# Kernel optimization log

Hardware: AMD Instinct MI355X
Metric: run time of the kernel (lower is better)

Reference implementation:

```python
import jax, jax.numpy as jnp
import numpy as np

B, S, D, H = 4, 2048, 1024, 16
DK = D // H

def setup_inputs() -> dict:
    key = jax.random.key(0)
    ks = jax.random.split(key, 5)
    scale = 1.0 / np.sqrt(D)
    return {
        "x": jax.random.normal(ks[0], (B, S, D), dtype=jnp.float32),
        "Wq": jax.random.normal(ks[1], (H, D, DK), dtype=jnp.float32) * scale,
        "Wk": jax.random.normal(ks[2], (H, D, DK), dtype=jnp.float32) * scale,
        "Wv": jax.random.normal(ks[3], (H, D, DK), dtype=jnp.float32) * scale,
        "Wo": jax.random.normal(ks[4], (D, D), dtype=jnp.float32) * scale,
    }

def reference(x, Wq, Wk, Wv, Wo):
    # x: [B,S,D]; Wq/Wk/Wv: [H,D,DK] (stacked per-head Linear weights); Wo: [D,D]
    seq = x.shape[-2]
    q = jnp.einsum('bsd,hdk->bhsk', x, Wq)
    k = jnp.einsum('bsd,hdk->bhsk', x, Wk)
    v = jnp.einsum('bsd,hdk->bhsk', x, Wv)
    dk = q.shape[-1]
    scores = jnp.einsum('bhqk,bhsk->bhqs', q, k) / jnp.sqrt(jnp.asarray(dk, x.dtype))
    # causal mask: mask out strictly-future positions (triu, diagonal=1)
    causal = jnp.tril(jnp.ones((seq, seq), dtype=bool))  # True = keep
    scores = jnp.where(causal, scores, -jnp.inf)
    probs = jax.nn.softmax(scores, axis=-1)  # attn_pdrop = 0.0 -> dropout is identity
    attn = jnp.einsum('bhqs,bhsk->bhqk', probs, v)
    # concat heads: [B,S,H*DK]
    concat = attn.transpose(0, 2, 1, 3).reshape(x.shape[0], seq, -1)
    # output_proj: nn.Linear(D, D, bias=False) -> y = concat @ Wo.T
    return jnp.einsum('bsd,ed->bse', concat, Wo)
```

## Files before the change

kernel.cpp:

```cpp
#include <hip/hip_runtime.h>
#include <hip/hip_bf16.h>

#define B_ 4
#define S_ 2048
#define D_ 1024
#define H_ 16
#define DK_ 64

typedef __attribute__((ext_vector_type(8))) short bf16x8;
typedef __attribute__((ext_vector_type(4))) float f32x4;
typedef __attribute__((ext_vector_type(4))) unsigned int u32x4;

__device__ __forceinline__ unsigned short f2bf(float f) {
    unsigned int u = __float_as_uint(f);
    u += 0x7FFFu + ((u >> 16) & 1u);
    return (unsigned short)(u >> 16);
}

__global__ void cvt_kernel(const float* __restrict__ src, unsigned short* __restrict__ dst) {
    int i = (blockIdx.x * 256 + threadIdx.x) * 8;
    float4 f0 = *(const float4*)&src[i];
    float4 f1 = *(const float4*)&src[i + 4];
    unsigned short t[8] __attribute__((aligned(16))) = {
        f2bf(f0.x), f2bf(f0.y), f2bf(f0.z), f2bf(f0.w),
        f2bf(f1.x), f2bf(f1.y), f2bf(f1.z), f2bf(f1.w)};
    *(u32x4*)&dst[i] = *(const u32x4*)t;
}

__global__ void prepack_kernel(const float* __restrict__ Wq,
                               const float* __restrict__ Wk,
                               const float* __restrict__ Wv,
                               unsigned short* __restrict__ Wt) {
    __shared__ unsigned short Ts[64 * 65];
    int h = blockIdx.x, w3 = blockIdx.y, t = blockIdx.z;
    const float* src = (w3 == 0 ? Wq : (w3 == 1 ? Wk : Wv)) + h * D_ * DK_ + t * 64 * DK_;
    unsigned short* dst = Wt + (w3 * H_ + h) * DK_ * D_ + t * 64;
    int tid = threadIdx.x;
    for (int rep = 0; rep < 16; ++rep) {
        int idx = rep * 256 + tid;
        int dl = idx >> 6, k = idx & 63;
        Ts[k * 65 + dl] = f2bf(src[dl * 64 + k]);
    }
    __syncthreads();
    for (int rep = 0; rep < 16; ++rep) {
        int idx = rep * 256 + tid;
        int kl = idx >> 6, dl = idx & 63;
        dst[kl * D_ + dl] = Ts[kl * 65 + dl];
    }
}

__device__ __forceinline__ void stage_tile_async(const unsigned short* __restrict__ g,
                                                 unsigned short* lds_base, int wv, int lane, int K) {
#pragma unroll
    for (int it = 0; it < 4; ++it) {
        int rbase = wv * 32 + it * 8;
        int r = rbase + (lane >> 3);
        int gc = (lane & 7) ^ ((lane >> 3) & 7);
        const unsigned short* gp = g + r * K + gc * 8;
        unsigned short* lp = lds_base + rbase * 64;
        __builtin_amdgcn_global_load_lds((const __attribute__((address_space(1))) unsigned int*)gp,
                                         (__attribute__((address_space(3))) unsigned int*)lp,
                                         16, 0, 0);
    }
}

template <bool QKV_OUT>
__global__ __launch_bounds__(256) void gemm128_kernel(const unsigned short* __restrict__ A,
                                                      const unsigned short* __restrict__ Bt,
                                                      void* __restrict__ Out) {
    __shared__ __align__(16) unsigned short As[128 * 64];
    __shared__ __align__(16) unsigned short Bs[128 * 64];
    const int tid = threadIdx.x;
    const int wv = tid >> 6, lane = tid & 63, l15 = lane & 15, q4 = lane >> 4;
    const int wm = wv >> 1, wn = wv & 1;
    const int r0 = blockIdx.x * 128, c0 = blockIdx.y * 128;

    const unsigned short* Ab = A + r0 * D_;
    const unsigned short* Bb = Bt + c0 * D_;

    f32x4 acc[4][4] = {};

    for (int kt = 0; kt < 16; ++kt) {
        stage_tile_async(Ab + kt * 64, As, wv, lane, D_);
        stage_tile_async(Bb + kt * 64, Bs, wv, lane, D_);
        __syncthreads();
#pragma unroll
        for (int kk = 0; kk < 2; ++kk) {
            bf16x8 af[4], bf[4];
            const int sw = ((kk * 4 + q4) ^ (l15 & 7)) * 8;
#pragma unroll
            for (int i = 0; i < 4; ++i) {
                af[i] = *(const bf16x8*)&As[(wm * 64 + i * 16 + l15) * 64 + sw];
                bf[i] = *(const bf16x8*)&Bs[(wn * 64 + i * 16 + l15) * 64 + sw];
            }
#pragma unroll
            for (int i = 0; i < 4; ++i)
#pragma unroll
                for (int j = 0; j < 4; ++j)
                    acc[i][j] = __builtin_amdgcn_mfma_f32_16x16x32_bf16(af[i], bf[j], acc[i][j], 0, 0, 0);
        }
        __syncthreads();
    }
#pragma unroll
    for (int i = 0; i < 4; ++i)
#pragma unroll
        for (int j = 0; j < 4; ++j)
#pragma unroll
            for (int rr = 0; rr < 4; ++rr) {
                int grow = r0 + wm * 64 + i * 16 + q4 * 4 + rr;
                int gcol = c0 + wn * 64 + j * 16 + l15;
                if (QKV_OUT) {
                    int b = grow >> 11, s = grow & (S_ - 1);
                    int w3 = gcol >> 10, h = (gcol >> 6) & 15, dk = gcol & 63;
                    ((unsigned short*)Out)[(((w3 * B_ + b) * H_ + h) * S_ + s) * DK_ + dk] =
                        f2bf(acc[i][j][rr]);
                } else {
                    ((float*)Out)[grow * D_ + gcol] = acc[i][j][rr];
                }
            }
}

__global__ __launch_bounds__(256, 4) void attn_kernel(const unsigned short* __restrict__ qkv,
                                                      unsigned short* __restrict__ concat) {
    const int pr = blockIdx.x;
    const int h = blockIdx.y, b = blockIdx.z;
    const unsigned short* Qp = qkv + ((0 * B_ + b) * H_ + h) * S_ * DK_;
    const unsigned short* Kp = qkv + ((1 * B_ + b) * H_ + h) * S_ * DK_;
    const unsigned short* Vp = qkv + ((2 * B_ + b) * H_ + h) * S_ * DK_;

    __shared__ __align__(16) unsigned short Ks[64 * 72];
    __shared__ __align__(16) unsigned short Vt[64 * 72];
    __shared__ __align__(16) __hip_bfloat16 Ps[4][16 * 72];

    const int tid = threadIdx.x;
    const int wv = tid >> 6, lane = tid & 63, l15 = lane & 15, q4 = lane >> 4;

    const float cs = 0.125f * 1.44269504088896340736f;
    const float MB = 16.0f;

    for (int side = 0; side < 2; ++side) {
        const int q0 = (side == 0 ? pr : 31 - pr) * 64;
        const int nk = q0 / 64 + 1;

        bf16x8 aq[2];
#pragma unroll
        for (int kk = 0; kk < 2; ++kk)
            aq[kk] = *(const bf16x8*)&Qp[(q0 + wv * 16 + l15) * DK_ + kk * 32 + q4 * 8];

        f32x4 o[4] = {};
        float l_[4] = {};

        for (int t = 0; t < nk; ++t) {
            const int k0 = t * 64;
#pragma unroll
            for (int it = 0; it < 2; ++it) {
                int c = it * 256 + tid;
                int row = c >> 3, ch = c & 7;
                *(u32x4*)&Ks[row * 72 + ch * 8] = *(const u32x4*)&Kp[(k0 + row) * DK_ + ch * 8];
                u32x4 vv = *(const u32x4*)&Vp[(k0 + row) * DK_ + ch * 8];
                const unsigned short* pv = (const unsigned short*)&vv;
#pragma unroll
                for (int j = 0; j < 8; ++j)
                    Vt[(ch * 8 + j) * 72 + (row ^ (ch * 8))] = pv[j];
            }
            __syncthreads();

            f32x4 sa[4] = {};
#pragma unroll
            for (int kk = 0; kk < 2; ++kk)
#pragma unroll
                for (int ct = 0; ct < 4; ++ct) {
                    bf16x8 bk = *(const bf16x8*)&Ks[(ct * 16 + l15) * 72 + kk * 32 + q4 * 8];
                    sa[ct] = __builtin_amdgcn_mfma_f32_16x16x32_bf16(aq[kk], bk, sa[ct], 0, 0, 0);
                }

            if (t < nk - 1) {
#pragma unroll
                for (int ct = 0; ct < 4; ++ct)
#pragma unroll
                    for (int r = 0; r < 4; r += 2) {
                        float p0 = exp2f(sa[ct][r] * cs - MB);
                        float p1 = exp2f(sa[ct][r + 1] * cs - MB);
                        l_[r] += p0;
                        l_[r + 1] += p1;
                        __hip_bfloat162 pk = __float22bfloat162_rn(make_float2(p0, p1));
                        Ps[wv][(q4 * 4 + r) * 72 + ct * 16 + l15] = pk.x;
                        Ps[wv][(q4 * 4 + r + 1) * 72 + ct * 16 + l15] = pk.y;
                    }
            } else {
                const int qrow_base = q0 + wv * 16 + q4 * 4;
#pragma unroll
                for (int ct = 0; ct < 4; ++ct) {
                    int col = k0 + ct * 16 + l15;
#pragma unroll
                    for (int r = 0; r < 4; r += 2) {
                        float a0 = (col <= qrow_base + r) ? sa[ct][r] * cs - MB : -1000.0f;
                        float a1 = (col <= qrow_base + r + 1) ? sa[ct][r + 1] * cs - MB : -1000.0f;
                        float p0 = exp2f(a0);
                        float p1 = exp2f(a1);
                        l_[r] += p0;
                        l_[r + 1] += p1;
                        __hip_bfloat162 pk = __float22bfloat162_rn(make_float2(p0, p1));
                        Ps[wv][(q4 * 4 + r) * 72 + ct * 16 + l15] = pk.x;
                        Ps[wv][(q4 * 4 + r + 1) * 72 + ct * 16 + l15] = pk.y;
                    }
                }
            }

#pragma unroll
            for (int kk = 0; kk < 2; ++kk) {
                bf16x8 ap = *(const bf16x8*)&Ps[wv][l15 * 72 + kk * 32 + q4 * 8];
#pragma unroll
                for (int cd = 0; cd < 4; ++cd) {
                    int drow = cd * 16 + l15;
                    int kbase = (kk * 32 + q4 * 8) ^ (drow & 56);
                    bf16x8 bv = *(const bf16x8*)&Vt[drow * 72 + kbase];
                    o[cd] = __builtin_amdgcn_mfma_f32_16x16x32_bf16(ap, bv, o[cd], 0, 0, 0);
                }
            }
            __syncthreads();
        }

#pragma unroll
        for (int r = 0; r < 4; ++r) {
            float lr = l_[r];
            lr += __shfl_xor(lr, 1);
            lr += __shfl_xor(lr, 2);
            lr += __shfl_xor(lr, 4);
            lr += __shfl_xor(lr, 8);
            float inv = 1.0f / fmaxf(lr, 1.0e-37f);
            int row = q0 + wv * 16 + q4 * 4 + r;
#pragma unroll
            for (int cd = 0; cd < 4; ++cd) {
                int col = h * DK_ + cd * 16 + l15;
                concat[(b * S_ + row) * D_ + col] = f2bf(o[cd][r] * inv);
            }
        }
    }
}

extern "C" void kernel_launch(void* const* d_in, const int* in_sizes, int n_in,
                              void* d_out, int out_size, void* d_ws, size_t ws_size,
                              hipStream_t stream) {
    const float* x  = (const float*)d_in[0];
    const float* Wq = (const float*)d_in[1];
    const float* Wk = (const float*)d_in[2];
    const float* Wv = (const float*)d_in[3];
    const float* Wo = (const float*)d_in[4];

    unsigned short* qkv    = (unsigned short*)d_ws;
    unsigned short* Wt     = qkv + 3 * B_ * H_ * S_ * DK_;
    unsigned short* xbf    = Wt + 3 * H_ * DK_ * D_;
    unsigned short* concat = xbf;
    unsigned short* Wobf   = Wt;

    cvt_kernel<<<B_ * S_ * D_ / 2048, 256, 0, stream>>>(x, xbf);
    prepack_kernel<<<dim3(H_, 3, 16), 256, 0, stream>>>(Wq, Wk, Wv, Wt);
    gemm128_kernel<true><<<dim3(B_ * S_ / 128, 3 * H_ * DK_ / 128), 256, 0, stream>>>(xbf, Wt, qkv);
    cvt_kernel<<<D_ * D_ / 2048, 256, 0, stream>>>(Wo, Wobf);
    attn_kernel<<<dim3(16, H_, B_), 256, 0, stream>>>(qkv, concat);
    gemm128_kernel<false><<<dim3(B_ * S_ / 128, D_ / 128), 256, 0, stream>>>(concat, Wobf, d_out);
}
```

Before: 279.0 us.

## Write V transposed from QKV GEMM and double-buffer async K/V loads in attention

The QKV projection GEMM now writes V already transposed ([b,h,dk,s]) through an LDS-staged swizzled tile, so the attention kernel no longer transposes V element by element in LDS. Attention stages K and Vt tiles with async global-to-LDS loads into double buffers, prefetching the next tile while computing the current one. It uses XOR swizzles instead of padded rows, and the grid is reordered so blocks for the same (b,h) are adjacent. This costs extra LDS and a more complex GEMM epilogue, and drops the occupancy hint on the attention kernel.

```diff
diff --git a/kernel.cpp b/kernel.cpp
--- a/kernel.cpp
+++ b/kernel.cpp
@@ -49,14 +49,14 @@
     }
 }
 
-__device__ __forceinline__ void stage_tile_async(const unsigned short* __restrict__ g,
-                                                 unsigned short* lds_base, int wv, int lane, int K) {
+__device__ __forceinline__ void stage128_async(const unsigned short* __restrict__ g,
+                                               unsigned short* lds_base, int wv, int lane, int ldg) {
 #pragma unroll
     for (int it = 0; it < 4; ++it) {
         int rbase = wv * 32 + it * 8;
         int r = rbase + (lane >> 3);
         int gc = (lane & 7) ^ ((lane >> 3) & 7);
-        const unsigned short* gp = g + r * K + gc * 8;
+        const unsigned short* gp = g + r * ldg + gc * 8;
         unsigned short* lp = lds_base + rbase * 64;
         __builtin_amdgcn_global_load_lds((const __attribute__((address_space(1))) unsigned int*)gp,
                                          (__attribute__((address_space(3))) unsigned int*)lp,
@@ -64,12 +64,29 @@
     }
 }
 
+__device__ __forceinline__ void stage64_async(const unsigned short* __restrict__ g,
+                                              unsigned short* lds_base, int wv, int lane, int ldg) {
+#pragma unroll
+    for (int it = 0; it < 2; ++it) {
+        int rbase = wv * 16 + it * 8;
+        int r = rbase + (lane >> 3);
+        int gc = (lane & 7) ^ ((lane >> 3) & 7);
+        const unsigned short* gp = g + r * ldg + gc * 8;
+        unsigned short* lp = lds_base + rbase * 64;
+        __builtin_amdgcn_global_load_lds((const __attribute__((address_space(1))) unsigned int*)gp,
+                                         (__attribute__((address_space(3))) unsigned int*)lp,
+                                         16, 0, 0);
+    }
+}
+
 template <bool QKV_OUT>
 __global__ __launch_bounds__(256) void gemm128_kernel(const unsigned short* __restrict__ A,
                                                       const unsigned short* __restrict__ Bt,
-                                                      void* __restrict__ Out) {
-    __shared__ __align__(16) unsigned short As[128 * 64];
-    __shared__ __align__(16) unsigned short Bs[128 * 64];
+                                                      void* __restrict__ Out,
+                                                      unsigned short* __restrict__ VtOut) {
+    __shared__ __align__(16) unsigned short smem[2 * 128 * 64];
+    unsigned short* As = smem;
+    unsigned short* Bs = smem + 128 * 64;
     const int tid = threadIdx.x;
     const int wv = tid >> 6, lane = tid & 63, l15 = lane & 15, q4 = lane >> 4;
     const int wm = wv >> 1, wn = wv & 1;
@@ -81,8 +98,8 @@
     f32x4 acc[4][4] = {};
 
     for (int kt = 0; kt < 16; ++kt) {
-        stage_tile_async(Ab + kt * 64, As, wv, lane, D_);
-        stage_tile_async(Bb + kt * 64, Bs, wv, lane, D_);
+        stage128_async(Ab + kt * 64, As, wv, lane, D_);
+        stage128_async(Bb + kt * 64, Bs, wv, lane, D_);
         __syncthreads();
 #pragma unroll
         for (int kk = 0; kk < 2; ++kk) {
@@ -101,36 +118,62 @@
         }
         __syncthreads();
     }
-#pragma unroll
-    for (int i = 0; i < 4; ++i)
-#pragma unroll
-        for (int j = 0; j < 4; ++j)
-#pragma unroll
-            for (int rr = 0; rr < 4; ++rr) {
-                int grow = r0 + wm * 64 + i * 16 + q4 * 4 + rr;
-                int gcol = c0 + wn * 64 + j * 16 + l15;
-                if (QKV_OUT) {
-                    int b = grow >> 11, s = grow & (S_ - 1);
-                    int w3 = gcol >> 10, h = (gcol >> 6) & 15, dk = gcol & 63;
-                    ((unsigned short*)Out)[(((w3 * B_ + b) * H_ + h) * S_ + s) * DK_ + dk] =
-                        f2bf(acc[i][j][rr]);
-                } else {
-                    ((float*)Out)[grow * D_ + gcol] = acc[i][j][rr];
-                }
-            }
-}
-
-__global__ __launch_bounds__(256, 4) void attn_kernel(const unsigned short* __restrict__ qkv,
-                                                      unsigned short* __restrict__ concat) {
-    const int pr = blockIdx.x;
-    const int h = blockIdx.y, b = blockIdx.z;
+
+    if (QKV_OUT && c0 >= 2 * D_) {
+        const int b = r0 >> 11, s0 = r0 & (S_ - 1);
+#pragma unroll
+        for (int i = 0; i < 4; ++i)
+#pragma unroll
+            for (int j = 0; j < 4; ++j)
+#pragma unroll
+                for (int rr = 0; rr < 4; ++rr) {
+                    int col = wn * 64 + j * 16 + l15;
+                    int row = wm * 64 + i * 16 + q4 * 4 + rr;
+                    smem[col * 128 + (row ^ ((col & 7) * 8))] = f2bf(acc[i][j][rr]);
+                }
+        __syncthreads();
+#pragma unroll
+        for (int rep = 0; rep < 8; ++rep) {
+            int idx = rep * 256 + tid;
+            int col = idx >> 4, ch = idx & 15;
+            u32x4 v = *(const u32x4*)&smem[col * 128 + ((ch * 8) ^ ((col & 7) * 8))];
+            int gcol = c0 + col;
+            int vrow = b * 1024 + (gcol & 1023);
+            *(u32x4*)&VtOut[vrow * S_ + s0 + ch * 8] = v;
+        }
+    } else {
+#pragma unroll
+        for (int i = 0; i < 4; ++i)
+#pragma unroll
+            for (int j = 0; j < 4; ++j)
+#pragma unroll
+                for (int rr = 0; rr < 4; ++rr) {
+                    int grow = r0 + wm * 64 + i * 16 + q4 * 4 + rr;
+                    int gcol = c0 + wn * 64 + j * 16 + l15;
+                    if (QKV_OUT) {
+                        int b = grow >> 11, s = grow & (S_ - 1);
+                        int w3 = gcol >> 10, h = (gcol >> 6) & 15, dk = gcol & 63;
+                        ((unsigned short*)Out)[(((w3 * B_ + b) * H_ + h) * S_ + s) * DK_ + dk] =
+                            f2bf(acc[i][j][rr]);
+                    } else {
+                        ((float*)Out)[grow * D_ + gcol] = acc[i][j][rr];
+                    }
+                }
+    }
+}
+
+__global__ __launch_bounds__(256) void attn_kernel(const unsigned short* __restrict__ qkv,
+                                                   unsigned short* __restrict__ concat) {
+    const int bh = blockIdx.x;
+    const int pr = blockIdx.y;
+    const int b = bh >> 4, h = bh & 15;
     const unsigned short* Qp = qkv + ((0 * B_ + b) * H_ + h) * S_ * DK_;
     const unsigned short* Kp = qkv + ((1 * B_ + b) * H_ + h) * S_ * DK_;
-    const unsigned short* Vp = qkv + ((2 * B_ + b) * H_ + h) * S_ * DK_;
-
-    __shared__ __align__(16) unsigned short Ks[64 * 72];
-    __shared__ __align__(16) unsigned short Vt[64 * 72];
-    __shared__ __align__(16) __hip_bfloat16 Ps[4][16 * 72];
+    const unsigned short* Vt = qkv + 2 * B_ * H_ * S_ * DK_ + (b * H_ + h) * DK_ * S_;
+
+    __shared__ __align__(16) unsigned short Kb[2][64 * 64];
+    __shared__ __align__(16) unsigned short Vb[2][64 * 64];
+    __shared__ __align__(16) unsigned short Ps[4][16 * 64];
 
     const int tid = threadIdx.x;
     const int wv = tid >> 6, lane = tid & 63, l15 = lane & 15, q4 = lane >> 4;
@@ -142,6 +185,9 @@
         const int q0 = (side == 0 ? pr : 31 - pr) * 64;
         const int nk = q0 / 64 + 1;
 
+        stage64_async(Kp + 0 * DK_, Kb[0], wv, lane, DK_);
+        stage64_async(Vt + 0, Vb[0], wv, lane, S_);
+
         bf16x8 aq[2];
 #pragma unroll
         for (int kk = 0; kk < 2; ++kk)
@@ -150,42 +196,37 @@
         f32x4 o[4] = {};
         float l_[4] = {};
 
+        __syncthreads();
+
         for (int t = 0; t < nk; ++t) {
             const int k0 = t * 64;
-#pragma unroll
-            for (int it = 0; it < 2; ++it) {
-                int c = it * 256 + tid;
-                int row = c >> 3, ch = c & 7;
-                *(u32x4*)&Ks[row * 72 + ch * 8] = *(const u32x4*)&Kp[(k0 + row) * DK_ + ch * 8];
-                u32x4 vv = *(const u32x4*)&Vp[(k0 + row) * DK_ + ch * 8];
-                const unsigned short* pv = (const unsigned short*)&vv;
-#pragma unroll
-                for (int j = 0; j < 8; ++j)
-                    Vt[(ch * 8 + j) * 72 + (row ^ (ch * 8))] = pv[j];
-            }
-            __syncthreads();
+            if (t + 1 < nk) {
+                stage64_async(Kp + (k0 + 64) * DK_, Kb[(t + 1) & 1], wv, lane, DK_);
+                stage64_async(Vt + (k0 + 64), Vb[(t + 1) & 1], wv, lane, S_);
+            }
+            const unsigned short* Kt = Kb[t & 1];
+            const unsigned short* Vtt = Vb[t & 1];
 
             f32x4 sa[4] = {};
 #pragma unroll
-            for (int kk = 0; kk < 2; ++kk)
+            for (int kk = 0; kk < 2; ++kk) {
+                const int sw = ((kk * 4 + q4) ^ (l15 & 7)) * 8;
 #pragma unroll
                 for (int ct = 0; ct < 4; ++ct) {
-                    bf16x8 bk = *(const bf16x8*)&Ks[(ct * 16 + l15) * 72 + kk * 32 + q4 * 8];
+                    bf16x8 bk = *(const bf16x8*)&Kt[(ct * 16 + l15) * 64 + sw];
                     sa[ct] = __builtin_amdgcn_mfma_f32_16x16x32_bf16(aq[kk], bk, sa[ct], 0, 0, 0);
                 }
+            }
 
             if (t < nk - 1) {
 #pragma unroll
                 for (int ct = 0; ct < 4; ++ct)
 #pragma unroll
-                    for (int r = 0; r < 4; r += 2) {
-                        float p0 = exp2f(sa[ct][r] * cs - MB);
-                        float p1 = exp2f(sa[ct][r + 1] * cs - MB);
-                        l_[r] += p0;
-                        l_[r + 1] += p1;
-                        __hip_bfloat162 pk = __float22bfloat162_rn(make_float2(p0, p1));
-                        Ps[wv][(q4 * 4 + r) * 72 + ct * 16 + l15] = pk.x;
-                        Ps[wv][(q4 * 4 + r + 1) * 72 + ct * 16 + l15] = pk.y;
+                    for (int r = 0; r < 4; ++r) {
+                        float p = exp2f(sa[ct][r] * cs - MB);
+                        l_[r] += p;
+                        int q = q4 * 4 + r;
+                        Ps[wv][q * 64 + ((ct * 16 + l15) ^ ((q & 7) * 8))] = f2bf(p);
                     }
             } else {
                 const int qrow_base = q0 + wv * 16 + q4 * 4;
@@ -193,28 +234,23 @@
                 for (int ct = 0; ct < 4; ++ct) {
                     int col = k0 + ct * 16 + l15;
 #pragma unroll
-                    for (int r = 0; r < 4; r += 2) {
-                        float a0 = (col <= qrow_base + r) ? sa[ct][r] * cs - MB : -1000.0f;
-                        float a1 = (col <= qrow_base + r + 1) ? sa[ct][r + 1] * cs - MB : -1000.0f;
-                        float p0 = exp2f(a0);
-                        float p1 = exp2f(a1);
-                        l_[r] += p0;
-                        l_[r + 1] += p1;
-                        __hip_bfloat162 pk = __float22bfloat162_rn(make_float2(p0, p1));
-                        Ps[wv][(q4 * 4 + r) * 72 + ct * 16 + l15] = pk.x;
-                        Ps[wv][(q4 * 4 + r + 1) * 72 + ct * 16 + l15] = pk.y;
+                    for (int r = 0; r < 4; ++r) {
+                        float a = (col <= qrow_base + r) ? sa[ct][r] * cs - MB : -1000.0f;
+                        float p = exp2f(a);
+                        l_[r] += p;
+                        int q = q4 * 4 + r;
+                        Ps[wv][q * 64 + ((ct * 16 + l15) ^ ((q & 7) * 8))] = f2bf(p);
                     }
                 }
             }
 
 #pragma unroll
             for (int kk = 0; kk < 2; ++kk) {
-                bf16x8 ap = *(const bf16x8*)&Ps[wv][l15 * 72 + kk * 32 + q4 * 8];
+                bf16x8 ap = *(const bf16x8*)&Ps[wv][l15 * 64 + ((kk * 32 + q4 * 8) ^ ((l15 & 7) * 8))];
+                const int sw = ((kk * 4 + q4) ^ (l15 & 7)) * 8;
 #pragma unroll
                 for (int cd = 0; cd < 4; ++cd) {
-                    int drow = cd * 16 + l15;
-                    int kbase = (kk * 32 + q4 * 8) ^ (drow & 56);
-                    bf16x8 bv = *(const bf16x8*)&Vt[drow * 72 + kbase];
+                    bf16x8 bv = *(const bf16x8*)&Vtt[(cd * 16 + l15) * 64 + sw];
                     o[cd] = __builtin_amdgcn_mfma_f32_16x16x32_bf16(ap, bv, o[cd], 0, 0, 0);
                 }
             }
@@ -253,11 +289,12 @@
     unsigned short* xbf    = Wt + 3 * H_ * DK_ * D_;
     unsigned short* concat = xbf;
     unsigned short* Wobf   = Wt;
+    unsigned short* VtOut  = qkv + 2 * B_ * H_ * S_ * DK_;
 
     cvt_kernel<<<B_ * S_ * D_ / 2048, 256, 0, stream>>>(x, xbf);
     prepack_kernel<<<dim3(H_, 3, 16), 256, 0, stream>>>(Wq, Wk, Wv, Wt);
-    gemm128_kernel<true><<<dim3(B_ * S_ / 128, 3 * H_ * DK_ / 128), 256, 0, stream>>>(xbf, Wt, qkv);
+    gemm128_kernel<true><<<dim3(B_ * S_ / 128, 3 * H_ * DK_ / 128), 256, 0, stream>>>(xbf, Wt, qkv, VtOut);
     cvt_kernel<<<D_ * D_ / 2048, 256, 0, stream>>>(Wo, Wobf);
-    attn_kernel<<<dim3(16, H_, B_), 256, 0, stream>>>(qkv, concat);
-    gemm128_kernel<false><<<dim3(B_ * S_ / 128, D_ / 128), 256, 0, stream>>>(concat, Wobf, d_out);
-}
+    attn_kernel<<<dim3(64, 16), 256, 0, stream>>>(qkv, concat);
+    gemm128_kernel<false><<<dim3(B_ * S_ / 128, D_ / 128), 256, 0, stream>>>(concat, Wobf, d_out, nullptr);
+}
```

Result: no change. 274.4 us (-1.7%).
